# Kernel optimization log

Hardware: AMD Instinct MI355X
Metric: run time of the kernel (lower is better)

Reference implementation:

```python
import jax, jax.numpy as jnp
import numpy as np
import math

NUM_HEADS = 16
HEAD_DIM = 64
DIM = 1024
IO_SLOTS = 16
NEG_INF = 1.0e9


def _alibi_slopes(num_heads):
    # slopes = ratio**i for i in 1..n, ratio = 2**(-8/n)
    ratio = 2.0 ** (-8.0 / num_heads)
    return jnp.array([ratio ** i for i in range(1, num_heads + 1)], dtype=jnp.float32)


def setup_inputs() -> dict:
    key = jax.random.key(0)
    ks = jax.random.split(key, 7)
    B, S, D = 2, 2048, DIM
    x = jax.random.normal(ks[0], (B, S, D), dtype=jnp.float32)
    is_getchar = jax.random.uniform(ks[1], (B, S), dtype=jnp.float32)
    is_putchar = jax.random.uniform(ks[2], (B, S), dtype=jnp.float32)
    scale = 0.02
    wq = jax.random.normal(ks[3], (D, NUM_HEADS * HEAD_DIM), dtype=jnp.float32) * scale
    wk = jax.random.normal(ks[4], (D, NUM_HEADS * HEAD_DIM), dtype=jnp.float32) * scale
    wv = jax.random.normal(ks[5], (D, NUM_HEADS * HEAD_DIM), dtype=jnp.float32) * scale
    wo = jax.random.normal(ks[6], (NUM_HEADS * HEAD_DIM, D), dtype=jnp.float32) * scale
    return {"x": x, "is_getchar": is_getchar, "is_putchar": is_putchar,
            "wq": wq, "wk": wk, "wv": wv, "wo": wo}


def reference(x, is_getchar, is_putchar, wq, wk, wv, wo):
    B, S, D = x.shape
    H, hd = NUM_HEADS, HEAD_DIM
    io_start = D - IO_SLOTS

    q = (x @ wq).reshape(B, S, H, hd)
    k = (x @ wk).reshape(B, S, H, hd)
    v = (x @ wv).reshape(B, S, H, hd)

    # scores[b,h,i,j] = q . k / sqrt(hd)
    scores = jnp.einsum("bihd,bjhd->bhij", q, k) / math.sqrt(hd)

    # standard ALiBi bias: -slope * (i - j), causal masked
    positions = jnp.arange(S)
    dist = (positions[:, None] - positions[None, :]).astype(jnp.float32)  # [S,S] = i - j
    slopes = _alibi_slopes(H)  # [H]
    bias = -slopes[:, None, None] * dist  # [H,S,S]
    causal = jnp.triu(jnp.ones((S, S), dtype=jnp.float32), k=1)
    bias = bias - causal * NEG_INF
    scores = scores + bias[None]

    # targeted read-head bias on head 0: -slope0 * |target - j|
    read_anchor = x[..., io_start + 0]  # [B,S]
    read_offset = x[..., io_start + 1]  # [B,S]
    target = read_anchor + 1.0 + read_offset  # [B,S]
    read_bias = -slopes[0] * jnp.abs(target[..., None] - positions.astype(jnp.float32))  # [B,S,S]
    head0 = jnp.where(is_getchar[:, None, :, None] > 0.5, read_bias[:, None], scores[:, :1])
    scores = scores.at[:, :1].set(head0)

    attn = jax.nn.softmax(scores, axis=-1)
    attn_out = jnp.einsum("bhij,bjhd->bihd", attn, v).reshape(B, S, H * hd)
    output = x + attn_out @ wo

    # I/O state updates (last 16 channels)
    output = output.at[..., io_start + 1].add(is_getchar)   # read_offset += getchar
    output = output.at[..., io_start + 3].add(is_putchar)   # write_offset += putchar
    output = output.at[..., io_start + 13].set(is_putchar)  # output_ready = putchar
    return output
```

## Files before the change

kernel.cpp:

```cpp
#include <hip/hip_runtime.h>
#include <hip/hip_bf16.h>

typedef __hip_bfloat16 bf16;
typedef __attribute__((ext_vector_type(8))) short short8;
typedef __attribute__((ext_vector_type(4))) short short4v;
typedef __attribute__((ext_vector_type(4))) float f32x4;

#define MFMA16(a, b, c) __builtin_amdgcn_mfma_f32_16x16x32_bf16((a), (b), (c), 0, 0, 0)

#if __has_builtin(__builtin_amdgcn_mfma_f32_16x16x16bf16_1k)
#define MFMA_PV(a, b, c) __builtin_amdgcn_mfma_f32_16x16x16bf16_1k((a), (b), (c), 0, 0, 0)
#elif __has_builtin(__builtin_amdgcn_mfma_f32_16x16x16_bf16)
#define MFMA_PV(a, b, c) __builtin_amdgcn_mfma_f32_16x16x16_bf16((a), (b), (c), 0, 0, 0)
#else
static __device__ __forceinline__ f32x4 mfma_pv_asm(short4v a, short4v b, f32x4 c) {
    f32x4 d;
    asm volatile("v_mfma_f32_16x16x16_bf16 %0, %1, %2, %3"
                 : "=&v"(d) : "v"(a), "v"(b), "v"(c));
    return d;
}
#define MFMA_PV(a, b, c) mfma_pv_asm((a), (b), (c))
#endif

static __device__ __forceinline__ void gload_lds16(const bf16* g, bf16* l) {
    __builtin_amdgcn_global_load_lds((const __attribute__((address_space(1))) void*)g,
                                     (__attribute__((address_space(3))) void*)l, 16, 0, 0);
}

__global__ __launch_bounds__(256) void prep_kernel(
    const float* __restrict__ x,
    const float* __restrict__ wq, const float* __restrict__ wk,
    const float* __restrict__ wv, const float* __restrict__ wo,
    bf16* __restrict__ Xb, bf16* __restrict__ WqkvT, bf16* __restrict__ WoT) {
    __shared__ bf16 tile[64][65];
    int bid = blockIdx.x;
    if (bid < 4096) {
        int i = (bid * 256 + threadIdx.x) * 4;
        float4 v = *(const float4*)(x + i);
        union { bf16 h4[4]; uint2 u; } p;
        p.h4[0] = __float2bfloat16(v.x);
        p.h4[1] = __float2bfloat16(v.y);
        p.h4[2] = __float2bfloat16(v.z);
        p.h4[3] = __float2bfloat16(v.w);
        *(uint2*)(Xb + i) = p.u;
        return;
    }
    int t2 = bid - 4096;
    int mat = t2 >> 8;
    int t   = t2 & 255;
    int tn  = t >> 4, tk = t & 15;
    const float* src = (mat == 0) ? wq : (mat == 1) ? wk : (mat == 2) ? wv : wo;
    bf16* dst = (mat < 3) ? (WqkvT + (size_t)mat * 1024 * 1024) : WoT;
    int tx = threadIdx.x & 63, ty = threadIdx.x >> 6;
    int k0 = tk * 64, n0 = tn * 64;
#pragma unroll
    for (int p = 0; p < 16; ++p) {
        int r = p * 4 + ty;
        tile[r][tx] = __float2bfloat16(src[(size_t)(k0 + r) * 1024 + n0 + tx]);
    }
    __syncthreads();
#pragma unroll
    for (int p = 0; p < 16; ++p) {
        int r = p * 4 + ty;
        dst[(size_t)(n0 + r) * 1024 + k0 + tx] = tile[tx][r];
    }
}

__global__ __launch_bounds__(256) void gemm_qkv_kernel(
    const bf16* __restrict__ A, const bf16* __restrict__ Bt,
    bf16* __restrict__ QK, bf16* __restrict__ Vt) {
    const int K = 1024;
    int bm = blockIdx.x, bn = blockIdx.y;
    __shared__ bf16 As[128 * 32];
    __shared__ bf16 Bs[128 * 32];
    int tid = threadIdx.x;
    int lane = tid & 63, w = tid >> 6;
    int wm = (w >> 1) * 64, wn = (w & 1) * 64;
    int q4 = lane >> 4, li = lane & 15;
    int srow = tid >> 2, sc = (tid & 3) * 8;

    const bf16* Ag = A + (size_t)(bm * 128 + srow) * K + sc;
    const bf16* Bg = Bt + (size_t)(bn * 128 + srow) * K + sc;
    bf16* Asl = As + tid * 8;
    bf16* Asl2 = As + 2048 + tid * 8;
    bf16* Bsl = Bs + tid * 8;
    bf16* Bsl2 = Bs + 2048 + tid * 8;

    f32x4 acc[4][4];
#pragma unroll
    for (int mt = 0; mt < 4; ++mt)
#pragma unroll
        for (int nt = 0; nt < 4; ++nt) acc[mt][nt] = (f32x4){0.f, 0.f, 0.f, 0.f};

    for (int k0 = 0; k0 < K; k0 += 32) {
        __syncthreads();
        gload_lds16(Ag + k0, Asl);
        gload_lds16(Ag + 64 * K + k0, Asl2);
        gload_lds16(Bg + k0, Bsl);
        gload_lds16(Bg + 64 * K + k0, Bsl2);
        __syncthreads();
        short8 af[4], bfb[4];
#pragma unroll
        for (int mt = 0; mt < 4; ++mt)
            af[mt] = *(const short8*)(As + (wm + mt * 16 + li) * 32 + q4 * 8);
#pragma unroll
        for (int nt = 0; nt < 4; ++nt)
            bfb[nt] = *(const short8*)(Bs + (wn + nt * 16 + li) * 32 + q4 * 8);
#pragma unroll
        for (int mt = 0; mt < 4; ++mt)
#pragma unroll
            for (int nt = 0; nt < 4; ++nt)
                acc[mt][nt] = MFMA16(af[mt], bfb[nt], acc[mt][nt]);
    }

    int rowb = bm * 128 + wm;
    if (bn < 16) {
        float qs = (bn < 8) ? 0.1803368801111244f : 1.0f;
#pragma unroll
        for (int mt = 0; mt < 4; ++mt) {
#pragma unroll
            for (int nt = 0; nt < 4; ++nt) {
                int col = bn * 128 + wn + nt * 16 + li;
#pragma unroll
                for (int r = 0; r < 4; ++r) {
                    int row = rowb + mt * 16 + q4 * 4 + r;
                    QK[(size_t)row * 2048 + col] = __float2bfloat16(acc[mt][nt][r] * qs);
                }
            }
        }
    } else {
#pragma unroll
        for (int mt = 0; mt < 4; ++mt) {
            int sbase = rowb + mt * 16 + q4 * 4;
            int b = sbase >> 11, s = sbase & 2047;
#pragma unroll
            for (int nt = 0; nt < 4; ++nt) {
                int n = bn * 128 + wn + nt * 16 + li - 2048;
                int h = n >> 6, d = n & 63;
                union { bf16 h4[4]; uint2 u; } pk;
#pragma unroll
                for (int r = 0; r < 4; ++r) pk.h4[r] = __float2bfloat16(acc[mt][nt][r]);
                *(uint2*)(Vt + (size_t)((b * 16 + h) * 64 + d) * 2048 + s) = pk.u;
            }
        }
    }
}

__global__ __launch_bounds__(256, 3) void attn_kernel(
    const bf16* __restrict__ QK, const bf16* __restrict__ Vt,
    const float* __restrict__ x, const float* __restrict__ gch,
    bf16* __restrict__ AO) {
    const int S = 2048;
    int idx = blockIdx.x;
    int ti, h, b;
    if (idx < 64) { h = 0; b = idx & 1; ti = idx >> 1; }
    else {
        int i2 = idx - 64;
        int row = i2 / 30;
        int j = i2 - row * 30;
        ti = 31 - row; h = 1 + (j >> 1); b = j & 1;
    }
    int i0 = ti * 64;
    int tid = threadIdx.x, lane = tid & 63, w = tid >> 6;
    int q4 = lane >> 4, li = lane & 15;

    __shared__ __align__(16) char smem[36864];
    bf16* Ks0 = (bf16*)(smem);
    bf16* Ks1 = (bf16*)(smem + 9216);
    bf16* Vs0 = (bf16*)(smem + 18432);
    bf16* Vs1 = (bf16*)(smem + 27648);
    float* Ored  = (float*)(smem);
    float* lsumB = (float*)(smem + 17408);

    short8 qf[4][2];
#pragma unroll
    for (int it = 0; it < 4; ++it) {
        const bf16* qp = QK + (size_t)(b * S + i0 + it * 16 + li) * 2048 + h * 64 + q4 * 8;
        qf[it][0] = *(const short8*)(qp);
        qf[it][1] = *(const short8*)(qp + 32);
    }

    const float L2E = 1.4426950408889634f;
    float sl1 = exp2f(-0.5f * (float)(h + 1)) * L2E;
    const float slope0L = 0.70710678118654752f * L2E;

    float tgt[4]; int gcm[4];
    if (h == 0) {
#pragma unroll
        for (int it = 0; it < 4; ++it) {
            size_t ix = (size_t)(b * S + i0 + it * 16 + li);
            gcm[it] = gch[ix] > 0.5f ? 1 : 0;
            tgt[it] = x[ix * 1024 + 1008] + 1.0f + x[ix * 1024 + 1009];
        }
    } else {
#pragma unroll
        for (int it = 0; it < 4; ++it) { gcm[it] = 0; tgt[it] = 0.f; }
    }

    float lsum[4] = {0.f, 0.f, 0.f, 0.f};
    f32x4 o[4][4];
#pragma unroll
    for (int it = 0; it < 4; ++it)
#pragma unroll
        for (int dt = 0; dt < 4; ++dt) o[it][dt] = (f32x4){0.f, 0.f, 0.f, 0.f};

    int srow = tid >> 3, scv = (tid & 7) * 8;
    const bf16* Kg = QK + (size_t)(b * S + srow) * 2048 + 1024 + h * 64 + scv;
    const bf16* Vg = Vt + (size_t)((b * 16 + h) * 64 + srow) * 2048 + scv;

    int ntiles = (h == 0) ? (S / 64) : (ti + 1);

    uint4 kv0 = *(const uint4*)(Kg);
    uint4 kv1 = *(const uint4*)(Kg + (size_t)32 * 2048);
    uint4 vv0 = *(const uint4*)(Vg);
    uint4 vv1 = *(const uint4*)(Vg + (size_t)32 * 2048);
    *(uint4*)(Ks0 + srow * 72 + scv) = kv0;
    *(uint4*)(Ks0 + (srow + 32) * 72 + scv) = kv1;
    *(uint4*)(Vs0 + srow * 72 + scv) = vv0;
    *(uint4*)(Vs0 + (srow + 32) * 72 + scv) = vv1;
    if (ntiles > 1) {
        kv0 = *(const uint4*)(Kg + (size_t)64 * 2048);
        kv1 = *(const uint4*)(Kg + (size_t)96 * 2048);
        vv0 = *(const uint4*)(Vg + 64);
        vv1 = *(const uint4*)(Vg + (size_t)32 * 2048 + 64);
    }
    __syncthreads();

    for (int jt = 0; jt < ntiles; ++jt) {
        const bf16* Kc = (jt & 1) ? Ks1 : Ks0;
        const bf16* Vc = (jt & 1) ? Vs1 : Vs0;
        if (jt + 1 < ntiles) {
            bf16* Kn = (jt & 1) ? Ks0 : Ks1;
            bf16* Vn = (jt & 1) ? Vs0 : Vs1;
            *(uint4*)(Kn + srow * 72 + scv) = kv0;
            *(uint4*)(Kn + (srow + 32) * 72 + scv) = kv1;
            *(uint4*)(Vn + srow * 72 + scv) = vv0;
            *(uint4*)(Vn + (srow + 32) * 72 + scv) = vv1;
            if (jt + 2 < ntiles) {
                size_t jn = (size_t)(jt + 2) * 64;
                kv0 = *(const uint4*)(Kg + jn * 2048);
                kv1 = *(const uint4*)(Kg + (jn + 32) * 2048);
                vv0 = *(const uint4*)(Vg + jn);
                vv1 = *(const uint4*)(Vg + (size_t)32 * 2048 + jn);
            }
        }

        int j0 = jt * 64;
        short8 kf0 = *(const short8*)(Kc + (w * 16 + li) * 72 + q4 * 8);
        short8 kf1 = *(const short8*)(Kc + (w * 16 + li) * 72 + 32 + q4 * 8);
        f32x4 sA[4];
#pragma unroll
        for (int it = 0; it < 4; ++it) {
            f32x4 z = (f32x4){0.f, 0.f, 0.f, 0.f};
            z = MFMA16(kf0, qf[it][0], z);
            z = MFMA16(kf1, qf[it][1], z);
            sA[it] = z;
        }

        float jbase = (float)(j0 + w * 16 + q4 * 4);
        bool diag = (jt >= ti);
        short4v pf[4];
#pragma unroll
        for (int it = 0; it < 4; ++it) {
            float fi = (float)(i0 + it * 16 + li);
            float d0 = jbase - fi;
            union { bf16 hh[4]; short4v v; } pu;
#pragma unroll
            for (int r = 0; r < 4; ++r) {
                float dj = d0 + (float)r;
                float p;
                if (h == 0) {
                    float s = fmaf(sl1, dj, sA[it][r]);
                    float sg = -slope0L * fabsf(tgt[it] - (jbase + (float)r));
                    s = gcm[it] ? sg : s;
                    p = exp2f(s);
                    if (!gcm[it] && dj > 0.f) p = 0.f;
                } else {
                    float s = fmaf(sl1, dj, sA[it][r]);
                    p = exp2f(s);
                    if (diag && dj > 0.f) p = 0.f;
                }
                lsum[it] += p;
                pu.hh[r] = __float2bfloat16(p);
            }
            pf[it] = pu.v;
        }

#pragma unroll
        for (int dt = 0; dt < 4; ++dt) {
            short4v vf = *(const short4v*)(Vc + (dt * 16 + li) * 72 + w * 16 + q4 * 4);
#pragma unroll
            for (int it = 0; it < 4; ++it)
                o[it][dt] = MFMA_PV(pf[it], vf, o[it][dt]);
        }
        __syncthreads();
    }

#pragma unroll
    for (int it = 0; it < 4; ++it) {
        lsum[it] += __shfl_xor(lsum[it], 16, 64);
        lsum[it] += __shfl_xor(lsum[it], 32, 64);
    }
    if (lane < 16) {
#pragma unroll
        for (int it = 0; it < 4; ++it) lsumB[w * 64 + it * 16 + lane] = lsum[it];
    }

    __syncthreads();
    if (w == 0) {
#pragma unroll
        for (int it = 0; it < 4; ++it)
#pragma unroll
            for (int dt = 0; dt < 4; ++dt)
#pragma unroll
                for (int r = 0; r < 4; ++r)
                    Ored[(it * 16 + q4 * 4 + r) * 68 + dt * 16 + li] = o[it][dt][r];
    }
    __syncthreads();
    if (w == 1) {
#pragma unroll
        for (int it = 0; it < 4; ++it)
#pragma unroll
            for (int dt = 0; dt < 4; ++dt)
#pragma unroll
                for (int r = 0; r < 4; ++r)
                    Ored[(it * 16 + q4 * 4 + r) * 68 + dt * 16 + li] += o[it][dt][r];
    }
    __syncthreads();
    if (w == 2) {
#pragma unroll
        for (int it = 0; it < 4; ++it)
#pragma unroll
            for (int dt = 0; dt < 4; ++dt)
#pragma unroll
                for (int r = 0; r < 4; ++r)
                    Ored[(it * 16 + q4 * 4 + r) * 68 + dt * 16 + li] += o[it][dt][r];
    }
    __syncthreads();
    if (w == 3) {
#pragma unroll
        for (int it = 0; it < 4; ++it)
#pragma unroll
            for (int dt = 0; dt < 4; ++dt)
#pragma unroll
                for (int r = 0; r < 4; ++r)
                    Ored[(it * 16 + q4 * 4 + r) * 68 + dt * 16 + li] += o[it][dt][r];
    }
    __syncthreads();

    int i = tid >> 2, dseg = (tid & 3) * 16;
    float ls = lsumB[i] + lsumB[64 + i] + lsumB[128 + i] + lsumB[192 + i];
    float inv = 1.0f / ls;
    bf16* dst = AO + (size_t)(b * S + i0 + i) * 1024 + h * 64 + dseg;
    union { bf16 hh[16]; uint4 u[2]; } ou;
#pragma unroll
    for (int c = 0; c < 16; ++c)
        ou.hh[c] = __float2bfloat16(Ored[i * 68 + dseg + c] * inv);
    *(uint4*)(dst) = ou.u[0];
    *(uint4*)(dst + 8) = ou.u[1];
}

__global__ __launch_bounds__(256) void gemm_out_kernel(
    const bf16* __restrict__ A, const bf16* __restrict__ Bt,
    const float* __restrict__ x, const float* __restrict__ gch,
    const float* __restrict__ pch, float* __restrict__ out) {
    const int K = 1024;
    int bm = blockIdx.x, bn = blockIdx.y;
    __shared__ bf16 As[128 * 32];
    __shared__ bf16 Bs[128 * 32];
    int tid = threadIdx.x;
    int lane = tid & 63, w = tid >> 6;
    int wm = (w >> 1) * 64, wn = (w & 1) * 64;
    int q4 = lane >> 4, li = lane & 15;
    int srow = tid >> 2, sc = (tid & 3) * 8;

    const bf16* Ag = A + (size_t)(bm * 128 + srow) * K + sc;
    const bf16* Bg = Bt + (size_t)(bn * 128 + srow) * K + sc;
    bf16* Asl = As + tid * 8;
    bf16* Asl2 = As + 2048 + tid * 8;
    bf16* Bsl = Bs + tid * 8;
    bf16* Bsl2 = Bs + 2048 + tid * 8;

    f32x4 acc[4][4];
#pragma unroll
    for (int mt = 0; mt < 4; ++mt)
#pragma unroll
        for (int nt = 0; nt < 4; ++nt) acc[mt][nt] = (f32x4){0.f, 0.f, 0.f, 0.f};

    for (int k0 = 0; k0 < K; k0 += 32) {
        __syncthreads();
        gload_lds16(Ag + k0, Asl);
        gload_lds16(Ag + 64 * K + k0, Asl2);
        gload_lds16(Bg + k0, Bsl);
        gload_lds16(Bg + 64 * K + k0, Bsl2);
        __syncthreads();
        short8 af[4], bfb[4];
#pragma unroll
        for (int mt = 0; mt < 4; ++mt)
            af[mt] = *(const short8*)(As + (wm + mt * 16 + li) * 32 + q4 * 8);
#pragma unroll
        for (int nt = 0; nt < 4; ++nt)
            bfb[nt] = *(const short8*)(Bs + (wn + nt * 16 + li) * 32 + q4 * 8);
#pragma unroll
        for (int mt = 0; mt < 4; ++mt)
#pragma unroll
            for (int nt = 0; nt < 4; ++nt)
                acc[mt][nt] = MFMA16(af[mt], bfb[nt], acc[mt][nt]);
    }

#pragma unroll
    for (int mt = 0; mt < 4; ++mt) {
#pragma unroll
        for (int nt = 0; nt < 4; ++nt) {
            int col = bn * 128 + wn + nt * 16 + li;
#pragma unroll
            for (int r = 0; r < 4; ++r) {
                int row = bm * 128 + wm + mt * 16 + q4 * 4 + r;
                size_t idx = (size_t)row * 1024 + col;
                float v = x[idx] + acc[mt][nt][r];
                if (col == 1009) v += gch[row];
                else if (col == 1011) v += pch[row];
                else if (col == 1021) v = pch[row];
                out[idx] = v;
            }
        }
    }
}

extern "C" void kernel_launch(void* const* d_in, const int* in_sizes, int n_in,
                              void* d_out, int out_size, void* d_ws, size_t ws_size,
                              hipStream_t stream) {
    (void)in_sizes; (void)n_in; (void)out_size; (void)ws_size;
    const float* x   = (const float*)d_in[0];
    const float* gch = (const float*)d_in[1];
    const float* pch = (const float*)d_in[2];
    const float* wq  = (const float*)d_in[3];
    const float* wk  = (const float*)d_in[4];
    const float* wv  = (const float*)d_in[5];
    const float* wo  = (const float*)d_in[6];
    float* out = (float*)d_out;

    char* ws = (char*)d_ws;
    bf16* Xb    = (bf16*)(ws);
    bf16* WqkvT = (bf16*)(ws + (size_t)( 8 << 20));
    bf16* WoT   = (bf16*)(ws + (size_t)(14 << 20));
    bf16* QK    = (bf16*)(ws + (size_t)(16 << 20));
    bf16* Vt    = (bf16*)(ws + (size_t)(32 << 20));
    bf16* AO    = Xb;

    prep_kernel<<<5120, 256, 0, stream>>>(x, wq, wk, wv, wo, Xb, WqkvT, WoT);
    gemm_qkv_kernel<<<dim3(32, 24), 256, 0, stream>>>(Xb, WqkvT, QK, Vt);
    attn_kernel<<<1024, 256, 0, stream>>>(QK, Vt, x, gch, AO);
    gemm_out_kernel<<<dim3(32, 8), 256, 0, stream>>>(AO, WoT, x, gch, pch, out);
}
```

Before: 212.2 us.

## Single-buffer attention LDS for higher occupancy and halve out-GEMM M tile

The attention kernel drops its double-buffered K/V shared memory and uses a single buffer with two barriers per tile, while still prefetching the next tile into registers. Launch bounds rise from 3 to 5 blocks per CU to use the freed LDS and registers. The softmax-probability code is split into separate unmasked, diagonal-masked and head-0 paths so off-diagonal tiles skip the mask compare. The output GEMM tile shrinks from 128x128 to 64x128, doubling the grid to fill more CUs, at the cost of an extra barrier per tile and more reloading of B in the GEMM.

```diff
diff --git a/kernel.cpp b/kernel.cpp
--- a/kernel.cpp
+++ b/kernel.cpp
@@ -146,7 +146,7 @@
     }
 }
 
-__global__ __launch_bounds__(256, 3) void attn_kernel(
+__global__ __launch_bounds__(256, 5) void attn_kernel(
     const bf16* __restrict__ QK, const bf16* __restrict__ Vt,
     const float* __restrict__ x, const float* __restrict__ gch,
     bf16* __restrict__ AO) {
@@ -164,11 +164,9 @@
     int tid = threadIdx.x, lane = tid & 63, w = tid >> 6;
     int q4 = lane >> 4, li = lane & 15;
 
-    __shared__ __align__(16) char smem[36864];
-    bf16* Ks0 = (bf16*)(smem);
-    bf16* Ks1 = (bf16*)(smem + 9216);
-    bf16* Vs0 = (bf16*)(smem + 18432);
-    bf16* Vs1 = (bf16*)(smem + 27648);
+    __shared__ __align__(16) char smem[18432];
+    bf16* Ks = (bf16*)(smem);
+    bf16* Vs = (bf16*)(smem + 9216);
     float* Ored  = (float*)(smem);
     float* lsumB = (float*)(smem + 17408);
 
@@ -205,49 +203,36 @@
         for (int dt = 0; dt < 4; ++dt) o[it][dt] = (f32x4){0.f, 0.f, 0.f, 0.f};
 
     int srow = tid >> 3, scv = (tid & 7) * 8;
-    const bf16* Kg = QK + (size_t)(b * S + srow) * 2048 + 1024 + h * 64 + scv;
-    const bf16* Vg = Vt + (size_t)((b * 16 + h) * 64 + srow) * 2048 + scv;
+    const bf16* Kp  = QK + (size_t)(b * S + srow) * 2048 + 1024 + h * 64 + scv;
+    const bf16* Kp2 = Kp + (size_t)32 * 2048;
+    const bf16* Vp  = Vt + (size_t)((b * 16 + h) * 64 + srow) * 2048 + scv;
+    const bf16* Vp2 = Vp + (size_t)32 * 2048;
 
     int ntiles = (h == 0) ? (S / 64) : (ti + 1);
 
-    uint4 kv0 = *(const uint4*)(Kg);
-    uint4 kv1 = *(const uint4*)(Kg + (size_t)32 * 2048);
-    uint4 vv0 = *(const uint4*)(Vg);
-    uint4 vv1 = *(const uint4*)(Vg + (size_t)32 * 2048);
-    *(uint4*)(Ks0 + srow * 72 + scv) = kv0;
-    *(uint4*)(Ks0 + (srow + 32) * 72 + scv) = kv1;
-    *(uint4*)(Vs0 + srow * 72 + scv) = vv0;
-    *(uint4*)(Vs0 + (srow + 32) * 72 + scv) = vv1;
-    if (ntiles > 1) {
-        kv0 = *(const uint4*)(Kg + (size_t)64 * 2048);
-        kv1 = *(const uint4*)(Kg + (size_t)96 * 2048);
-        vv0 = *(const uint4*)(Vg + 64);
-        vv1 = *(const uint4*)(Vg + (size_t)32 * 2048 + 64);
-    }
-    __syncthreads();
+    uint4 kv0 = *(const uint4*)(Kp);
+    uint4 kv1 = *(const uint4*)(Kp2);
+    uint4 vv0 = *(const uint4*)(Vp);
+    uint4 vv1 = *(const uint4*)(Vp2);
+    Kp += 131072; Kp2 += 131072; Vp += 64; Vp2 += 64;
 
     for (int jt = 0; jt < ntiles; ++jt) {
-        const bf16* Kc = (jt & 1) ? Ks1 : Ks0;
-        const bf16* Vc = (jt & 1) ? Vs1 : Vs0;
+        __syncthreads();
+        *(uint4*)(Ks + srow * 72 + scv) = kv0;
+        *(uint4*)(Ks + (srow + 32) * 72 + scv) = kv1;
+        *(uint4*)(Vs + srow * 72 + scv) = vv0;
+        *(uint4*)(Vs + (srow + 32) * 72 + scv) = vv1;
+        __syncthreads();
         if (jt + 1 < ntiles) {
-            bf16* Kn = (jt & 1) ? Ks0 : Ks1;
-            bf16* Vn = (jt & 1) ? Vs0 : Vs1;
-            *(uint4*)(Kn + srow * 72 + scv) = kv0;
-            *(uint4*)(Kn + (srow + 32) * 72 + scv) = kv1;
-            *(uint4*)(Vn + srow * 72 + scv) = vv0;
-            *(uint4*)(Vn + (srow + 32) * 72 + scv) = vv1;
-            if (jt + 2 < ntiles) {
-                size_t jn = (size_t)(jt + 2) * 64;
-                kv0 = *(const uint4*)(Kg + jn * 2048);
-                kv1 = *(const uint4*)(Kg + (jn + 32) * 2048);
-                vv0 = *(const uint4*)(Vg + jn);
-                vv1 = *(const uint4*)(Vg + (size_t)32 * 2048 + jn);
-            }
-        }
-
-        int j0 = jt * 64;
-        short8 kf0 = *(const short8*)(Kc + (w * 16 + li) * 72 + q4 * 8);
-        short8 kf1 = *(const short8*)(Kc + (w * 16 + li) * 72 + 32 + q4 * 8);
+            kv0 = *(const uint4*)(Kp);
+            kv1 = *(const uint4*)(Kp2);
+            vv0 = *(const uint4*)(Vp);
+            vv1 = *(const uint4*)(Vp2);
+            Kp += 131072; Kp2 += 131072; Vp += 64; Vp2 += 64;
+        }
+
+        short8 kf0 = *(const short8*)(Ks + (w * 16 + li) * 72 + q4 * 8);
+        short8 kf1 = *(const short8*)(Ks + (w * 16 + li) * 72 + 32 + q4 * 8);
         f32x4 sA[4];
 #pragma unroll
         for (int it = 0; it < 4; ++it) {
@@ -257,43 +242,65 @@
             sA[it] = z;
         }
 
-        float jbase = (float)(j0 + w * 16 + q4 * 4);
-        bool diag = (jt >= ti);
+        float jbase = (float)(jt * 64 + w * 16 + q4 * 4);
         short4v pf[4];
-#pragma unroll
-        for (int it = 0; it < 4; ++it) {
-            float fi = (float)(i0 + it * 16 + li);
-            float d0 = jbase - fi;
-            union { bf16 hh[4]; short4v v; } pu;
-#pragma unroll
-            for (int r = 0; r < 4; ++r) {
-                float dj = d0 + (float)r;
-                float p;
-                if (h == 0) {
+        if (h != 0) {
+            if (jt < ti) {
+#pragma unroll
+                for (int it = 0; it < 4; ++it) {
+                    float d0 = jbase - (float)(i0 + it * 16 + li);
+                    union { bf16 hh[4]; short4v v; } pu;
+#pragma unroll
+                    for (int r = 0; r < 4; ++r) {
+                        float p = exp2f(fmaf(sl1, d0 + (float)r, sA[it][r]));
+                        lsum[it] += p;
+                        pu.hh[r] = __float2bfloat16(p);
+                    }
+                    pf[it] = pu.v;
+                }
+            } else {
+#pragma unroll
+                for (int it = 0; it < 4; ++it) {
+                    float d0 = jbase - (float)(i0 + it * 16 + li);
+                    union { bf16 hh[4]; short4v v; } pu;
+#pragma unroll
+                    for (int r = 0; r < 4; ++r) {
+                        float dj = d0 + (float)r;
+                        float p = exp2f(fmaf(sl1, dj, sA[it][r]));
+                        if (dj > 0.f) p = 0.f;
+                        lsum[it] += p;
+                        pu.hh[r] = __float2bfloat16(p);
+                    }
+                    pf[it] = pu.v;
+                }
+            }
+        } else {
+#pragma unroll
+            for (int it = 0; it < 4; ++it) {
+                float d0 = jbase - (float)(i0 + it * 16 + li);
+                union { bf16 hh[4]; short4v v; } pu;
+#pragma unroll
+                for (int r = 0; r < 4; ++r) {
+                    float dj = d0 + (float)r;
                     float s = fmaf(sl1, dj, sA[it][r]);
                     float sg = -slope0L * fabsf(tgt[it] - (jbase + (float)r));
                     s = gcm[it] ? sg : s;
-                    p = exp2f(s);
+                    float p = exp2f(s);
                     if (!gcm[it] && dj > 0.f) p = 0.f;
-                } else {
-                    float s = fmaf(sl1, dj, sA[it][r]);
-                    p = exp2f(s);
-                    if (diag && dj > 0.f) p = 0.f;
+                    lsum[it] += p;
+                    pu.hh[r] = __float2bfloat16(p);
                 }
-                lsum[it] += p;
-                pu.hh[r] = __float2bfloat16(p);
+                pf[it] = pu.v;
             }
-            pf[it] = pu.v;
         }
 
 #pragma unroll
         for (int dt = 0; dt < 4; ++dt) {
-            short4v vf = *(const short4v*)(Vc + (dt * 16 + li) * 72 + w * 16 + q4 * 4);
+            short4v vf = *(const short4v*)(Vs + (dt * 16 + li) * 72 + w * 16 + q4 * 4);
 #pragma unroll
             for (int it = 0; it < 4; ++it)
                 o[it][dt] = MFMA_PV(pf[it], vf, o[it][dt]);
         }
-        __syncthreads();
     }
 
 #pragma unroll
@@ -301,12 +308,11 @@
         lsum[it] += __shfl_xor(lsum[it], 16, 64);
         lsum[it] += __shfl_xor(lsum[it], 32, 64);
     }
+    __syncthreads();
     if (lane < 16) {
 #pragma unroll
         for (int it = 0; it < 4; ++it) lsumB[w * 64 + it * 16 + lane] = lsum[it];
     }
-
-    __syncthreads();
     if (w == 0) {
 #pragma unroll
         for (int it = 0; it < 4; ++it)
@@ -366,56 +372,54 @@
     const float* __restrict__ pch, float* __restrict__ out) {
     const int K = 1024;
     int bm = blockIdx.x, bn = blockIdx.y;
-    __shared__ bf16 As[128 * 32];
+    __shared__ bf16 As[64 * 32];
     __shared__ bf16 Bs[128 * 32];
     int tid = threadIdx.x;
     int lane = tid & 63, w = tid >> 6;
-    int wm = (w >> 1) * 64, wn = (w & 1) * 64;
+    int wm = (w & 1) * 32, wn = (w >> 1) * 64;
     int q4 = lane >> 4, li = lane & 15;
     int srow = tid >> 2, sc = (tid & 3) * 8;
 
-    const bf16* Ag = A + (size_t)(bm * 128 + srow) * K + sc;
+    const bf16* Ag = A + (size_t)(bm * 64 + srow) * K + sc;
     const bf16* Bg = Bt + (size_t)(bn * 128 + srow) * K + sc;
     bf16* Asl = As + tid * 8;
-    bf16* Asl2 = As + 2048 + tid * 8;
     bf16* Bsl = Bs + tid * 8;
     bf16* Bsl2 = Bs + 2048 + tid * 8;
 
-    f32x4 acc[4][4];
-#pragma unroll
-    for (int mt = 0; mt < 4; ++mt)
+    f32x4 acc[2][4];
+#pragma unroll
+    for (int mt = 0; mt < 2; ++mt)
 #pragma unroll
         for (int nt = 0; nt < 4; ++nt) acc[mt][nt] = (f32x4){0.f, 0.f, 0.f, 0.f};
 
     for (int k0 = 0; k0 < K; k0 += 32) {
         __syncthreads();
         gload_lds16(Ag + k0, Asl);
-        gload_lds16(Ag + 64 * K + k0, Asl2);
         gload_lds16(Bg + k0, Bsl);
         gload_lds16(Bg + 64 * K + k0, Bsl2);
         __syncthreads();
-        short8 af[4], bfb[4];
-#pragma unroll
-        for (int mt = 0; mt < 4; ++mt)
+        short8 af[2], bfb[4];
+#pragma unroll
+        for (int mt = 0; mt < 2; ++mt)
             af[mt] = *(const short8*)(As + (wm + mt * 16 + li) * 32 + q4 * 8);
 #pragma unroll
         for (int nt = 0; nt < 4; ++nt)
             bfb[nt] = *(const short8*)(Bs + (wn + nt * 16 + li) * 32 + q4 * 8);
 #pragma unroll
-        for (int mt = 0; mt < 4; ++mt)
+        for (int mt = 0; mt < 2; ++mt)
 #pragma unroll
             for (int nt = 0; nt < 4; ++nt)
                 acc[mt][nt] = MFMA16(af[mt], bfb[nt], acc[mt][nt]);
     }
 
 #pragma unroll
-    for (int mt = 0; mt < 4; ++mt) {
+    for (int mt = 0; mt < 2; ++mt) {
 #pragma unroll
         for (int nt = 0; nt < 4; ++nt) {
             int col = bn * 128 + wn + nt * 16 + li;
 #pragma unroll
             for (int r = 0; r < 4; ++r) {
-                int row = bm * 128 + wm + mt * 16 + q4 * 4 + r;
+                int row = bm * 64 + wm + mt * 16 + q4 * 4 + r;
                 size_t idx = (size_t)row * 1024 + col;
                 float v = x[idx] + acc[mt][nt][r];
                 if (col == 1009) v += gch[row];
@@ -451,5 +455,5 @@
     prep_kernel<<<5120, 256, 0, stream>>>(x, wq, wk, wv, wo, Xb, WqkvT, WoT);
     gemm_qkv_kernel<<<dim3(32, 24), 256, 0, stream>>>(Xb, WqkvT, QK, Vt);
     attn_kernel<<<1024, 256, 0, stream>>>(QK, Vt, x, gch, AO);
-    gemm_out_kernel<<<dim3(32, 8), 256, 0, stream>>>(AO, WoT, x, gch, pch, out);
-}
+    gemm_out_kernel<<<dim3(64, 8), 256, 0, stream>>>(AO, WoT, x, gch, pch, out);
+}
```

Result: slower. 539.1 us (+154.0%).
